# Performance work log

Measured on AMD Instinct MI355X. Metric: run time of the kernel, lower is better.

The kernel has to match this reference:

```python
import jax, jax.numpy as jnp
import numpy as np

B, N, CT, CS, CP, H, NB = 1, 1024, 768, 384, 16, 16, 4
DH = CT // H
NL, NK = 8, 32          # n_local_tokens, n_keys
K = NL + NK
SCALE = 1.0 / np.sqrt(DH)


def _ln(x, g=None, b=None, eps=1e-5):
    m = jnp.mean(x, -1, keepdims=True)
    v = jnp.var(x, -1, keepdims=True)
    y = (x - m) * jax.lax.rsqrt(v + eps)
    if g is not None:
        y = y * g
    if b is not None:
        y = y + b
    return y


def _adaln(a, s, sln_g, sw, sb, shw):
    # AF3 AdaLN: a <- sigmoid(Lin(s_n)) * LN(a) + LinNoBias(s_n)
    an = _ln(a)
    sn = _ln(s, sln_g)
    return jax.nn.sigmoid(sn @ sw + sb) * an + sn @ shw


def _indices(X_L):
    # n_local sequence neighbours (clamped window) + n_keys spatial nearest
    off = jnp.arange(NL) - NL // 2
    loc = jnp.clip(jnp.arange(N)[:, None] + off[None, :], 0, N - 1)  # [N,NL]
    d2 = jnp.sum((X_L[:, :, None, :] - X_L[:, None, :, :]) ** 2, -1)  # [B,N,N]
    _, nk = jax.lax.top_k(-d2, NK)                                    # [B,N,NK]
    loc = jnp.broadcast_to(loc[None], (X_L.shape[0], N, NL))
    return jnp.concatenate([loc, nk], -1)                             # [B,N,K]


def setup_inputs() -> dict:
    key = jax.random.key(0)
    ks = list(jax.random.split(key, 24))
    f32 = jnp.float32

    def rn(k, shape, s=0.02):
        return (jax.random.normal(k, shape) * s).astype(f32)

    d = {}
    d['A_I'] = jax.random.normal(ks[0], (B, N, CT), f32)
    d['S_I'] = jax.random.normal(ks[1], (B, N, CS), f32)
    d['Z_II'] = jax.random.normal(ks[2], (B, N, N, CP), f32)
    d['X_L'] = jax.random.normal(ks[3], (B, N, 3), f32) * 10.0
    d['f'] = jax.random.randint(ks[4], (B, N), 0, 4)
    # attention-pair-bias block params (stacked over NB blocks)
    d['aln1_sln_g'] = jnp.ones((NB, CS), f32)
    d['aln1_sw'] = rn(ks[5], (NB, CS, CT))
    d['aln1_sb'] = jnp.zeros((NB, CT), f32)
    d['aln1_shw'] = rn(ks[6], (NB, CS, CT))
    d['Wq'] = rn(ks[7], (NB, CT, CT))
    d['bq'] = jnp.zeros((NB, CT), f32)
    d['Wk'] = rn(ks[8], (NB, CT, CT))
    d['Wv'] = rn(ks[9], (NB, CT, CT))
    d['pair_ln_g'] = jnp.ones((NB, CP), f32)
    d['pair_ln_b'] = jnp.zeros((NB, CP), f32)
    d['Wb'] = rn(ks[10], (NB, CP, H))
    d['Wg'] = rn(ks[11], (NB, CT, CT))
    d['Wo'] = rn(ks[12], (NB, CT, CT))
    d['sg_w'] = rn(ks[13], (NB, CS, CT))
    d['sg_b'] = jnp.full((NB, CT), -2.0, f32)   # LinearBiasInit(-2.0)
    # conditioned transition block params
    d['aln2_sln_g'] = jnp.ones((NB, CS), f32)
    d['aln2_sw'] = rn(ks[14], (NB, CS, CT))
    d['aln2_sb'] = jnp.zeros((NB, CT), f32)
    d['aln2_shw'] = rn(ks[15], (NB, CS, CT))
    d['t_w1'] = rn(ks[16], (NB, CT, 2 * CT))
    d['t_w2'] = rn(ks[17], (NB, CT, 2 * CT))
    d['t_w3'] = rn(ks[18], (NB, 2 * CT, CT))
    d['tsg_w'] = rn(ks[19], (NB, CS, CT))
    d['tsg_b'] = jnp.full((NB, CT), -2.0, f32)
    return d


def reference(A_I, S_I, Z_II, X_L, f,
              aln1_sln_g, aln1_sw, aln1_sb, aln1_shw,
              Wq, bq, Wk, Wv, pair_ln_g, pair_ln_b, Wb, Wg, Wo, sg_w, sg_b,
              aln2_sln_g, aln2_sw, aln2_sb, aln2_shw,
              t_w1, t_w2, t_w3, tsg_w, tsg_b):
    idx = _indices(X_L)                       # [B,N,K] int
    bb = jnp.arange(B)[:, None, None]
    nn_ = jnp.arange(N)[None, :, None]
    zg = Z_II[bb, nn_, idx]                   # [B,N,K,CP] gathered pair reps
    A = A_I
    for i in range(NB):
        # LocalAttentionPairBias
        an = _adaln(A, S_I, aln1_sln_g[i], aln1_sw[i], aln1_sb[i], aln1_shw[i])
        q = (an @ Wq[i] + bq[i]).reshape(B, N, H, DH)
        kg = (an @ Wk[i])[bb, idx].reshape(B, N, K, H, DH)
        vg = (an @ Wv[i])[bb, idx].reshape(B, N, K, H, DH)
        bias = _ln(zg, pair_ln_g[i], pair_ln_b[i]) @ Wb[i]      # [B,N,K,H]
        sc = jnp.einsum('bnhd,bnkhd->bnhk', q, kg) * SCALE + jnp.swapaxes(bias, -1, -2)
        w = jax.nn.softmax(sc, -1)                               # [B,N,H,K]
        o = jnp.einsum('bnhk,bnkhd->bnhd', w, vg).reshape(B, N, CT)
        o = jax.nn.sigmoid(an @ Wg[i]) * o                       # per-channel gate
        o = jax.nn.sigmoid(S_I @ sg_w[i] + sg_b[i]) * (o @ Wo[i])
        A = A + o                                                # dropout=0 (eval)
        # ConditionedTransitionBlock (SwiGLU, n=2)
        an2 = _adaln(A, S_I, aln2_sln_g[i], aln2_sw[i], aln2_sb[i], aln2_shw[i])
        hb = jax.nn.silu(an2 @ t_w1[i]) * (an2 @ t_w2[i])
        A = A + jax.nn.sigmoid(S_I @ tsg_w[i] + tsg_b[i]) * (hb @ t_w3[i])
    return A
```

## Files before the change

### kernel.cpp

```cpp
#include <hip/hip_runtime.h>
#include <hip/hip_bf16.h>
#include <math.h>
#include <stdint.h>

#define NTOK 1024
#define CT   768
#define CS   384
#define CP   16
#define NH   16
#define DH   48
#define NBLK 4
#define NL   8
#define NKEY 32
#define KTOT 40
#define SCALE_ 0.14433756729740643f

#define WS_BLK      8257536
#define OFF_A1SW    0
#define OFF_A1SHW   294912
#define OFF_QKVG    589824
#define OFF_WO      2949120
#define OFF_SGT     3538944
#define OFF_A2SW    4128768
#define OFF_A2SHW   4423680
#define OFF_TW1     4718592
#define OFF_TW2     5898240
#define OFF_TW3     7077888

typedef __attribute__((ext_vector_type(8))) short short8;
typedef __attribute__((ext_vector_type(4))) float f32x4;
typedef __attribute__((ext_vector_type(4))) unsigned int u32x4;

#define AS1 __attribute__((address_space(1)))
#define AS3 __attribute__((address_space(3)))

__device__ __forceinline__ float sigmoidf_(float x) {
    return 1.0f / (1.0f + __expf(-x));
}
__device__ __forceinline__ float bf2f(unsigned short u) {
    union { unsigned int i; float f; } v; v.i = (unsigned int)u << 16; return v.f;
}
__device__ __forceinline__ unsigned short f2bf(float f) {
    return __bfloat16_as_ushort(__float2bfloat16(f));
}

__device__ __forceinline__ void gl_lds16(const void* g, void* l) {
    __builtin_amdgcn_global_load_lds((const AS1 void*)(uintptr_t)g,
                                     (AS3 void*)(uintptr_t)l, 16, 0, 0);
}

__global__ __launch_bounds__(256)
void topk_kernel(const float* __restrict__ X, int* __restrict__ idx) {
    const int w = threadIdx.x >> 6;
    const int l = threadIdx.x & 63;
    const int n = blockIdx.x * 4 + w;

    const float x0 = X[n * 3 + 0], x1 = X[n * 3 + 1], x2 = X[n * 3 + 2];
    float d[16];
    unsigned long long lkey = ~0ull;
#pragma unroll
    for (int j = 0; j < 16; ++j) {
        int m = j * 64 + l;
        float dx = x0 - X[m * 3 + 0];
        float dy = x1 - X[m * 3 + 1];
        float dz = x2 - X[m * 3 + 2];
        float v = dx * dx + dy * dy + dz * dz;
        d[j] = v;
        unsigned long long key =
            ((unsigned long long)__float_as_uint(v) << 32) | (unsigned int)m;
        lkey = key < lkey ? key : lkey;
    }
    if (l < NL) {
        int loc = n + l - NL / 2;
        loc = loc < 0 ? 0 : (loc > NTOK - 1 ? NTOK - 1 : loc);
        idx[n * KTOT + l] = loc;
    }

    for (int it = 0; it < NKEY; ++it) {
        unsigned long long rk = lkey;
#pragma unroll
        for (int s = 32; s > 0; s >>= 1) {
            unsigned long long o = __shfl_xor(rk, s, 64);
            rk = o < rk ? o : rk;
        }
        unsigned int win = (unsigned int)rk;
        if (l == 0) idx[n * KTOT + NL + it] = (int)win;
        if ((int)(win & 63) == l) {
            int jw = (int)(win >> 6);
            unsigned long long nk = ~0ull;
#pragma unroll
            for (int j = 0; j < 16; ++j) {
                if (j == jw) d[j] = INFINITY;
                unsigned long long key =
                    ((unsigned long long)__float_as_uint(d[j]) << 32) |
                    (unsigned int)(j * 64 + l);
                nk = key < nk ? key : nk;
            }
            lkey = nk;
        }
    }
}

__global__ __launch_bounds__(384)
void sprep_kernel(const float* __restrict__ S, const float* __restrict__ g1,
                  const float* __restrict__ g2,
                  __hip_bfloat16* __restrict__ S_bf,
                  __hip_bfloat16* __restrict__ snb) {
    int r = blockIdx.x, t = threadIdx.x;
    int wid = t >> 6, l = t & 63;
    __shared__ float ls[12];
    float v = S[r * CS + t];
    float s = v;
#pragma unroll
    for (int m = 32; m > 0; m >>= 1) s += __shfl_xor(s, m, 64);
    if (l == 0) ls[wid] = s;
    __syncthreads();
    float mean = (ls[0] + ls[1] + ls[2] + ls[3] + ls[4] + ls[5]) * (1.0f / CS);
    float d = v - mean;
    float q = d * d;
#pragma unroll
    for (int m = 32; m > 0; m >>= 1) q += __shfl_xor(q, m, 64);
    if (l == 0) ls[6 + wid] = q;
    __syncthreads();
    float rstd = rsqrtf((ls[6] + ls[7] + ls[8] + ls[9] + ls[10] + ls[11]) *
                        (1.0f / CS) + 1e-5f);
    float ln = d * rstd;
    S_bf[r * CS + t] = __float2bfloat16(v);
#pragma unroll
    for (int j = 0; j < 8; ++j) {
        const float* g = ((j & 1) ? g2 : g1) + (j >> 1) * CS;
        snb[((size_t)j * NTOK + r) * CS + t] = __float2bfloat16(ln * g[t]);
    }
}

__global__ __launch_bounds__(256)
void adaapply_kernel(const float* __restrict__ A,
                     const __hip_bfloat16* __restrict__ SIG,
                     const __hip_bfloat16* __restrict__ SH,
                     __hip_bfloat16* __restrict__ an) {
    int r = blockIdx.x, t = threadIdx.x;
    int wid = t >> 6, l = t & 63;
    __shared__ float ls[8];
    const float* ar = A + (size_t)r * CT;
    float v0 = ar[t], v1 = ar[t + 256], v2 = ar[t + 512];
    float s = v0 + v1 + v2;
#pragma unroll
    for (int m = 32; m > 0; m >>= 1) s += __shfl_xor(s, m, 64);
    if (l == 0) ls[wid] = s;
    __syncthreads();
    float mean = (ls[0] + ls[1] + ls[2] + ls[3]) * (1.0f / CT);
    float d0 = v0 - mean, d1 = v1 - mean, d2 = v2 - mean;
    float q = d0 * d0 + d1 * d1 + d2 * d2;
#pragma unroll
    for (int m = 32; m > 0; m >>= 1) q += __shfl_xor(q, m, 64);
    if (l == 0) ls[4 + wid] = q;
    __syncthreads();
    float rstd = rsqrtf((ls[4] + ls[5] + ls[6] + ls[7]) * (1.0f / CT) + 1e-5f);
    size_t base = (size_t)r * CT;
    float dd[3] = {d0, d1, d2};
#pragma unroll
    for (int k = 0; k < 3; ++k) {
        int c = t + k * 256;
        float sg = sigmoidf_(__bfloat162float(SIG[base + c]));
        float sh = __bfloat162float(SH[base + c]);
        an[base + c] = __float2bfloat16(sg * dd[k] * rstd + sh);
    }
}

struct ConvDesc { const float* src; __hip_bfloat16* dst; int K; int N; int tstart; int srcStride; };
struct ConvTable { ConvDesc e[14]; };

__global__ __launch_bounds__(256)
void convT_kernel(ConvTable tab) {
    int b = blockIdx.x;
    int ei = 0;
#pragma unroll
    for (int j = 1; j < 14; ++j) if (b >= tab.e[j].tstart) ei = j;
    ConvDesc d = tab.e[ei];
    const float* src = d.src + (size_t)blockIdx.y * d.srcStride;
    unsigned short* dst = (unsigned short*)(d.dst + (size_t)blockIdx.y * WS_BLK);
    int tt = b - d.tstart;
    int ntn = d.N / 64;
    int k0 = (tt / ntn) * 128, n0 = (tt % ntn) * 64;

    __shared__ __align__(16) unsigned int lbT[64 * 64];
    const int t = threadIdx.x;
    const int nq = (t & 15) * 4;

    f32x4 va[4], vc[4];
#pragma unroll
    for (int it = 0; it < 4; ++it) {
        int k = ((t >> 4) + it * 16) * 2;
        va[it] = *(const f32x4*)&src[(size_t)(k0 + k) * d.N + n0 + nq];
        vc[it] = *(const f32x4*)&src[(size_t)(k0 + k + 1) * d.N + n0 + nq];
    }
#pragma unroll
    for (int it = 0; it < 4; ++it) {
        int k2 = (t >> 4) + it * 16;
#pragma unroll
        for (int j = 0; j < 4; ++j) {
            int n = nq + j;
            unsigned int u = (unsigned int)f2bf(va[it][j]) |
                             ((unsigned int)f2bf(vc[it][j]) << 16);
            lbT[n * 64 + (k2 ^ (((n >> 1) & 15) << 2))] = u;
        }
    }
    __syncthreads();
#pragma unroll
    for (int it = 0; it < 4; ++it) {
        int task = t + it * 256;
        int n = task >> 4;
        int kcg = task & 15;
        int k2s = (kcg * 4) ^ (((n >> 1) & 15) << 2);
        u32x4 v = *(const u32x4*)&lbT[n * 64 + k2s];
        *(u32x4*)&dst[(size_t)(n0 + n) * d.K + k0 + kcg * 8] = v;
    }
}

__global__ __launch_bounds__(256)
void biasprep_kernel(const float* __restrict__ bq, const float* __restrict__ sg_b,
                     const float* __restrict__ tsg_b, float* __restrict__ qb,
                     float* __restrict__ sb2) {
    int t = blockIdx.x * 256 + threadIdx.x;
    if (t < NBLK * 3072) {
        int i = t / 3072, c = t % 3072;
        qb[t] = (c < 768) ? bq[i * 768 + c] : 0.0f;
    }
    if (t < NBLK * 1536) {
        int i = t / 1536, c = t % 1536;
        sb2[t] = (c < 768) ? sg_b[i * 768 + c] : tsg_b[i * 768 + c - 768];
    }
}

template <int MODE>
__global__ __launch_bounds__(256)
void gemmw_kernel(const __hip_bfloat16* A, const __hip_bfloat16* B1,
                  const float* cb1, const float* cb2,
                  __hip_bfloat16* outb, __hip_bfloat16* outb2,
                  int K, int N, int ldo) {
    __shared__ __align__(16) char As[2][16384];
    __shared__ __align__(16) char Bs[2][8192];

    const float* cb = cb1;
    __hip_bfloat16* outp = outb;
    if constexpr (MODE == 5) {
        int z = blockIdx.z;
        int j = z & 7, half = z >> 3;
        A += (size_t)j * NTOK * CS;
        B1 += (size_t)(j >> 1) * WS_BLK + ((j & 1) ? OFF_A2SW : OFF_A1SW)
            + (size_t)half * (OFF_A1SHW - OFF_A1SW);
        cb = half ? nullptr : (((j & 1) ? cb2 : cb1) + (j >> 1) * CT);
        outp = (half ? outb2 : outb) + (size_t)j * NTOK * CT;
    } else if constexpr (MODE == 6) {
        int z = blockIdx.z;
        B1 += (size_t)z * WS_BLK;
        cb = cb1 + z * 1536;
        outp = outb + (size_t)z * NTOK * 1536;
    }

    const int tid = threadIdx.x;
    const int lane = tid & 63;
    const int wid = tid >> 6;
    const int row0 = blockIdx.y * 128;
    const int col0 = blockIdx.x * 64;

    const int srow = tid >> 3;
    const int sg_e = (((tid & 7) ^ (srow & 7)) << 3);
    const __hip_bfloat16* ag = A + (size_t)(row0 + srow) * K + sg_e;
    const __hip_bfloat16* bg = B1 + (size_t)(col0 + srow) * K + sg_e;
    const size_t r32K = (size_t)32 * K;

    auto STAGE = [&](int bi) {
        char* al = As[bi] + tid * 16;
        char* bl = Bs[bi] + tid * 16;
        gl_lds16(ag, al);
        gl_lds16(ag + r32K, al + 4096);
        gl_lds16(ag + 2 * r32K, al + 8192);
        gl_lds16(ag + 3 * r32K, al + 12288);
        gl_lds16(bg, bl);
        gl_lds16(bg + r32K, bl + 4096);
        ag += 64; bg += 64;
    };

    f32x4 acc[2][4];
#pragma unroll
    for (int i = 0; i < 2; ++i)
#pragma unroll
        for (int j = 0; j < 4; ++j) acc[i][j] = (f32x4){0.f, 0.f, 0.f, 0.f};

    const int l15 = lane & 15;
    const int lhi = lane >> 4;
    const int nIter = K >> 6;

    STAGE(0);
    for (int it = 0; it < nIter; ++it) {
        __syncthreads();
        if (it + 1 < nIter) STAGE((it + 1) & 1);
        const char* Ab = As[it & 1];
        const char* Bb = Bs[it & 1];
#pragma unroll
        for (int kk = 0; kk < 2; ++kk) {
            const int c = lhi + 4 * kk;
            short8 a[2], bv[4];
#pragma unroll
            for (int mi = 0; mi < 2; ++mi) {
                int ra = wid * 32 + mi * 16 + l15;
                a[mi] = *(const short8*)(Ab + ra * 128 + (((c ^ (ra & 7)) << 4)));
            }
#pragma unroll
            for (int ni = 0; ni < 4; ++ni) {
                int rb = ni * 16 + l15;
                bv[ni] = *(const short8*)(Bb + rb * 128 + (((c ^ (rb & 7)) << 4)));
            }
#pragma unroll
            for (int mi = 0; mi < 2; ++mi)
#pragma unroll
                for (int ni = 0; ni < 4; ++ni)
                    acc[mi][ni] = __builtin_amdgcn_mfma_f32_16x16x32_bf16(
                        a[mi], bv[ni], acc[mi][ni], 0, 0, 0);
        }
    }

#pragma unroll
    for (int mi = 0; mi < 2; ++mi)
#pragma unroll
        for (int ni = 0; ni < 4; ++ni) {
            int col = col0 + ni * 16 + l15;
            int rbase = row0 + wid * 32 + mi * 16 + lhi * 4;
            float cbv = cb ? cb[col] : 0.0f;
            f32x4 v = acc[mi][ni];
#pragma unroll
            for (int r = 0; r < 4; ++r)
                outp[(size_t)(rbase + r) * ldo + col] = __float2bfloat16(v[r] + cbv);
        }
}

template <int MODE>
__global__ __launch_bounds__(256)
void gemm_kernel(const __hip_bfloat16* __restrict__ A,
                 const __hip_bfloat16* B1,
                 const __hip_bfloat16* B2,
                 const __hip_bfloat16* __restrict__ auxb, int ld_aux,
                 float* __restrict__ outf,
                 __hip_bfloat16* outb,
                 int K, int N, int ldo) {
    constexpr bool DUAL = (MODE == 2);
    __shared__ __align__(16) char As[2][8192];
    __shared__ __align__(16) char Bs[2][8192];
    __shared__ __align__(16) char Bs2[DUAL ? 2 : 1][DUAL ? 8192 : 16];

    const int tid = threadIdx.x;
    const int lane = tid & 63;
    const int wid = tid >> 6;
    const int wr = wid >> 1, wc = wid & 1;
    const int row0 = blockIdx.y * 64;
    const int col0 = blockIdx.x * 64;

    const int srow = tid >> 3;
    const int sg_e = (((tid & 7) ^ (srow & 7)) << 3);
    const __hip_bfloat16* ag = A + (size_t)(row0 + srow) * K + sg_e;
    const __hip_bfloat16* bg = B1 + (size_t)(col0 + srow) * K + sg_e;
    const __hip_bfloat16* bg2 = DUAL ? (B2 + (size_t)(col0 + srow) * K + sg_e) : nullptr;
    const size_t r32K = (size_t)32 * K;

    auto STAGE = [&](int bi) {
        gl_lds16(ag, As[bi] + tid * 16);
        gl_lds16(ag + r32K, As[bi] + 4096 + tid * 16);
        gl_lds16(bg, Bs[bi] + tid * 16);
        gl_lds16(bg + r32K, Bs[bi] + 4096 + tid * 16);
        if (DUAL) {
            gl_lds16(bg2, Bs2[bi] + tid * 16);
            gl_lds16(bg2 + r32K, Bs2[bi] + 4096 + tid * 16);
            bg2 += 64;
        }
        ag += 64; bg += 64;
    };

    f32x4 acc[2][2];
    f32x4 acc2[2][2];
#pragma unroll
    for (int i = 0; i < 2; ++i)
#pragma unroll
        for (int j = 0; j < 2; ++j) {
            acc[i][j] = (f32x4){0.f, 0.f, 0.f, 0.f};
            acc2[i][j] = (f32x4){0.f, 0.f, 0.f, 0.f};
        }

    const int l15 = lane & 15;
    const int lhi = lane >> 4;
    const int nIter = K >> 6;

    STAGE(0);
    for (int it = 0; it < nIter; ++it) {
        __syncthreads();
        if (it + 1 < nIter) STAGE((it + 1) & 1);
        const char* Ab = As[it & 1];
        const char* Bb = Bs[it & 1];
        const char* Cb = DUAL ? Bs2[it & 1] : nullptr;
#pragma unroll
        for (int kk = 0; kk < 2; ++kk) {
            const int c = lhi + 4 * kk;
            const int ra0 = wr * 32 + l15, ra1 = ra0 + 16;
            const int rb0 = wc * 32 + l15, rb1 = rb0 + 16;
            short8 a0 = *(const short8*)(Ab + ra0 * 128 + (((c ^ (ra0 & 7)) << 4)));
            short8 a1 = *(const short8*)(Ab + ra1 * 128 + (((c ^ (ra1 & 7)) << 4)));
            short8 b0 = *(const short8*)(Bb + rb0 * 128 + (((c ^ (rb0 & 7)) << 4)));
            short8 b1 = *(const short8*)(Bb + rb1 * 128 + (((c ^ (rb1 & 7)) << 4)));
            acc[0][0] = __builtin_amdgcn_mfma_f32_16x16x32_bf16(a0, b0, acc[0][0], 0, 0, 0);
            acc[0][1] = __builtin_amdgcn_mfma_f32_16x16x32_bf16(a0, b1, acc[0][1], 0, 0, 0);
            acc[1][0] = __builtin_amdgcn_mfma_f32_16x16x32_bf16(a1, b0, acc[1][0], 0, 0, 0);
            acc[1][1] = __builtin_amdgcn_mfma_f32_16x16x32_bf16(a1, b1, acc[1][1], 0, 0, 0);
            if (DUAL) {
                short8 c0 = *(const short8*)(Cb + rb0 * 128 + (((c ^ (rb0 & 7)) << 4)));
                short8 c1 = *(const short8*)(Cb + rb1 * 128 + (((c ^ (rb1 & 7)) << 4)));
                acc2[0][0] = __builtin_amdgcn_mfma_f32_16x16x32_bf16(a0, c0, acc2[0][0], 0, 0, 0);
                acc2[0][1] = __builtin_amdgcn_mfma_f32_16x16x32_bf16(a0, c1, acc2[0][1], 0, 0, 0);
                acc2[1][0] = __builtin_amdgcn_mfma_f32_16x16x32_bf16(a1, c0, acc2[1][0], 0, 0, 0);
                acc2[1][1] = __builtin_amdgcn_mfma_f32_16x16x32_bf16(a1, c1, acc2[1][1], 0, 0, 0);
            }
        }
    }

#pragma unroll
    for (int mi = 0; mi < 2; ++mi)
#pragma unroll
        for (int ni = 0; ni < 2; ++ni) {
            f32x4 v1 = acc[mi][ni];
            f32x4 v2 = acc2[mi][ni];
            int col = col0 + wc * 32 + ni * 16 + l15;
            int rbase = row0 + wr * 32 + mi * 16 + lhi * 4;
#pragma unroll
            for (int r = 0; r < 4; ++r) {
                int row = rbase + r;
                size_t o = (size_t)row * ldo + col;
                if (MODE == 2) {
                    float x = v1[r];
                    outb[o] = __float2bfloat16(x * sigmoidf_(x) * v2[r]);
                } else {
                    float g = sigmoidf_(__bfloat162float(auxb[(size_t)row * ld_aux + col]));
                    outf[o] += g * v1[r];
                }
            }
        }
}

__global__ __launch_bounds__(256)
void attn_kernel(const __hip_bfloat16* __restrict__ qkvg,
                 const float* __restrict__ Z,
                 const int* __restrict__ idx,
                 const float* __restrict__ pg, const float* __restrict__ pb,
                 const float* __restrict__ Wbp,
                 __hip_bfloat16* __restrict__ o2) {
    int n = blockIdx.x;
    int t = threadIdx.x;
    __shared__ __align__(16) unsigned short qs[768];
    __shared__ float sc[16][48];
    __shared__ float lnz[KTOT][16];
    __shared__ float wb[16][17];
    __shared__ float pgs[16], pbs[16];
    __shared__ int sidx[KTOT];

    wb[t >> 4][t & 15] = Wbp[t];
    if (t < 96) ((short8*)qs)[t] = ((const short8*)(qkvg + (size_t)n * 3072))[t];
    if (t >= 96 && t < 96 + KTOT) sidx[t - 96] = idx[n * KTOT + (t - 96)];
    if (t >= 160 && t < 176) pgs[t - 160] = pg[t - 160];
    if (t >= 176 && t < 192) pbs[t - 176] = pb[t - 176];
    __syncthreads();

    if (t < KTOT) {
        const f32x4* z = (const f32x4*)(Z + ((size_t)n * NTOK + sidx[t]) * CP);
        f32x4 z0 = z[0], z1 = z[1], z2 = z[2], z3 = z[3];
        float v[16];
#pragma unroll
        for (int e = 0; e < 4; ++e) { v[e] = z0[e]; v[4 + e] = z1[e]; v[8 + e] = z2[e]; v[12 + e] = z3[e]; }
        float s = 0.0f;
#pragma unroll
        for (int c = 0; c < 16; ++c) s += v[c];
        float mean = s * (1.0f / 16.0f);
        float s2 = 0.0f;
#pragma unroll
        for (int c = 0; c < 16; ++c) { float d = v[c] - mean; s2 += d * d; }
        float rstd = rsqrtf(s2 * (1.0f / 16.0f) + 1e-5f);
#pragma unroll
        for (int c = 0; c < 16; ++c) lnz[t][c] = (v[c] - mean) * rstd * pgs[c] + pbs[c];
    }
    __syncthreads();

    for (int task = t; task < NH * KTOT; task += 256) {
        int h = task / KTOT, k = task - h * KTOT;
        const short8* kp = (const short8*)((const unsigned short*)qkvg +
                                           (size_t)sidx[k] * 3072 + 768 + h * DH);
        const short8* qp = (const short8*)(qs + h * DH);
        float s = 0.0f;
#pragma unroll
        for (int j = 0; j < 6; ++j) {
            short8 kv = kp[j];
            short8 qv = qp[j];
#pragma unroll
            for (int e = 0; e < 8; ++e)
                s += bf2f((unsigned short)qv[e]) * bf2f((unsigned short)kv[e]);
        }
        float bias = 0.0f;
#pragma unroll
        for (int c = 0; c < 16; ++c) bias += lnz[k][c] * wb[c][h];
        sc[h][k] = s * SCALE_ + bias;
    }
    __syncthreads();

    {
        int h = t >> 4, l = t & 15;
        float v0 = sc[h][l];
        float v1 = sc[h][l + 16];
        float v2 = (l < 8) ? sc[h][l + 32] : -INFINITY;
        float mx = fmaxf(fmaxf(v0, v1), v2);
#pragma unroll
        for (int m = 8; m > 0; m >>= 1) mx = fmaxf(mx, __shfl_xor(mx, m, 16));
        float e0 = __expf(v0 - mx), e1 = __expf(v1 - mx);
        float e2 = (l < 8) ? __expf(v2 - mx) : 0.0f;
        float sm = e0 + e1 + e2;
#pragma unroll
        for (int m = 8; m > 0; m >>= 1) sm += __shfl_xor(sm, m, 16);
        float inv = 1.0f / sm;
        sc[h][l] = e0 * inv;
        sc[h][l + 16] = e1 * inv;
        if (l < 8) sc[h][l + 32] = e2 * inv;
    }
    __syncthreads();

    if (t < 96) {
        int h = t / 6, c6 = t - h * 6;
        int d0 = c6 * 8;
        const unsigned short* vbase = (const unsigned short*)qkvg + 1536 + h * DH + d0;
        float acc[8] = {0, 0, 0, 0, 0, 0, 0, 0};
        for (int k = 0; k < KTOT; ++k) {
            short8 vv = *(const short8*)(vbase + (size_t)sidx[k] * 3072);
            float w = sc[h][k];
#pragma unroll
            for (int e = 0; e < 8; ++e) acc[e] += w * bf2f((unsigned short)vv[e]);
        }
        short8 gv = *(const short8*)((const unsigned short*)qkvg +
                                     (size_t)n * 3072 + 2304 + h * DH + d0);
        short8 ov;
#pragma unroll
        for (int e = 0; e < 8; ++e) {
            float g = sigmoidf_(bf2f((unsigned short)gv[e]));
            ov[e] = (short)f2bf(g * acc[e]);
        }
        *(short8*)((unsigned short*)o2 + (size_t)n * CT + h * DH + d0) = ov;
    }
}

extern "C" void kernel_launch(void* const* d_in, const int* in_sizes, int n_in,
                              void* d_out, int out_size, void* d_ws, size_t ws_size,
                              hipStream_t stream) {
    const float* A_I  = (const float*)d_in[0];
    const float* S_I  = (const float*)d_in[1];
    const float* Z_II = (const float*)d_in[2];
    const float* X_L  = (const float*)d_in[3];
    const float* aln1_sln_g = (const float*)d_in[5];
    const float* aln1_sw    = (const float*)d_in[6];
    const float* aln1_sb    = (const float*)d_in[7];
    const float* aln1_shw   = (const float*)d_in[8];
    const float* Wq  = (const float*)d_in[9];
    const float* bq  = (const float*)d_in[10];
    const float* Wk  = (const float*)d_in[11];
    const float* Wv  = (const float*)d_in[12];
    const float* pair_ln_g = (const float*)d_in[13];
    const float* pair_ln_b = (const float*)d_in[14];
    const float* Wbp = (const float*)d_in[15];
    const float* Wg  = (const float*)d_in[16];
    const float* Wo  = (const float*)d_in[17];
    const float* sg_w = (const float*)d_in[18];
    const float* sg_b = (const float*)d_in[19];
    const float* aln2_sln_g = (const float*)d_in[20];
    const float* aln2_sw    = (const float*)d_in[21];
    const float* aln2_sb    = (const float*)d_in[22];
    const float* aln2_shw   = (const float*)d_in[23];
    const float* t_w1 = (const float*)d_in[24];
    const float* t_w2 = (const float*)d_in[25];
    const float* t_w3 = (const float*)d_in[26];
    const float* tsg_w = (const float*)d_in[27];
    const float* tsg_b = (const float*)d_in[28];
    (void)in_sizes; (void)n_in; (void)out_size; (void)ws_size;

    float* A = (float*)d_out;

    char* ws = (char*)d_ws;
    size_t off = 0;
    auto alloc = [&](size_t bytes) {
        void* p = ws + off;
        off += (bytes + 255) & ~(size_t)255;
        return p;
    };
    int*   idx    = (int*)  alloc(NTOK * KTOT * 4);
    __hip_bfloat16* S_bf  = (__hip_bfloat16*)alloc((size_t)NTOK * CS * 2);
    __hip_bfloat16* snb   = (__hip_bfloat16*)alloc((size_t)8 * NTOK * CS * 2);
    __hip_bfloat16* an    = (__hip_bfloat16*)alloc((size_t)NTOK * CT * 2);
    __hip_bfloat16* qkvg  = (__hip_bfloat16*)alloc((size_t)NTOK * 3072 * 2);
    __hip_bfloat16* sgateb= (__hip_bfloat16*)alloc((size_t)NBLK * NTOK * 1536 * 2);
    __hip_bfloat16* SIG   = (__hip_bfloat16*)alloc((size_t)8 * NTOK * CT * 2);
    __hip_bfloat16* SH    = (__hip_bfloat16*)alloc((size_t)8 * NTOK * CT * 2);
    __hip_bfloat16* o2    = (__hip_bfloat16*)alloc((size_t)NTOK * CT * 2);
    __hip_bfloat16* hb    = (__hip_bfloat16*)alloc((size_t)NTOK * 2 * CT * 2);
    float* qkvgbias = (float*)alloc((size_t)NBLK * 3072 * 4);
    float* sgbias   = (float*)alloc((size_t)NBLK * 1536 * 4);
    __hip_bfloat16* Wbuf = (__hip_bfloat16*)alloc((size_t)NBLK * WS_BLK * 2);

    hipMemcpyAsync(A, A_I, (size_t)NTOK * CT * 4, hipMemcpyDeviceToDevice, stream);

    topk_kernel<<<NTOK / 4, 256, 0, stream>>>(X_L, idx);
    sprep_kernel<<<NTOK, 384, 0, stream>>>(S_I, aln1_sln_g, aln2_sln_g, S_bf, snb);
    biasprep_kernel<<<NBLK * 3072 / 256, 256, 0, stream>>>(bq, sg_b, tsg_b, qkvgbias, sgbias);

    {
        ConvTable tab;
        int p = 0, ts = 0;
        auto add = [&](const float* s, size_t dstOff, int Kk, int Nn, int sstride) {
            tab.e[p].src = s; tab.e[p].dst = Wbuf + dstOff; tab.e[p].K = Kk;
            tab.e[p].N = Nn; tab.e[p].tstart = ts; tab.e[p].srcStride = sstride;
            ts += (Kk / 128) * (Nn / 64); ++p;
        };
        add(aln1_sw,  OFF_A1SW,           384, 768,  CS * CT);
        add(aln1_shw, OFF_A1SHW,          384, 768,  CS * CT);
        add(Wq, OFF_QKVG + 0 * 589824,    768, 768,  CT * CT);
        add(Wk, OFF_QKVG + 1 * 589824,    768, 768,  CT * CT);
        add(Wv, OFF_QKVG + 2 * 589824,    768, 768,  CT * CT);
        add(Wg, OFF_QKVG + 3 * 589824,    768, 768,  CT * CT);
        add(Wo, OFF_WO,                   768, 768,  CT * CT);
        add(sg_w,  OFF_SGT,               384, 768,  CS * CT);
        add(tsg_w, OFF_SGT + 768 * 384,   384, 768,  CS * CT);
        add(aln2_sw,  OFF_A2SW,           384, 768,  CS * CT);
        add(aln2_shw, OFF_A2SHW,          384, 768,  CS * CT);
        add(t_w1, OFF_TW1,                768, 1536, CT * 2 * CT);
        add(t_w2, OFF_TW2,                768, 1536, CT * 2 * CT);
        add(t_w3, OFF_TW3,                1536, 768, 2 * CT * CT);
        convT_kernel<<<dim3(ts, NBLK), 256, 0, stream>>>(tab);
    }

    gemmw_kernel<5><<<dim3(12, 8, 16), 256, 0, stream>>>(
        snb, Wbuf, aln1_sb, aln2_sb, SIG, SH, 384, 768, 768);
    gemmw_kernel<6><<<dim3(24, 8, 4), 256, 0, stream>>>(
        S_bf, Wbuf + OFF_SGT, sgbias, nullptr, sgateb, nullptr, 384, 1536, 1536);

    for (int i = 0; i < NBLK; ++i) {
        const __hip_bfloat16* Wb_i = Wbuf + (size_t)i * WS_BLK;
        __hip_bfloat16* sg_i = sgateb + (size_t)i * NTOK * 1536;

        adaapply_kernel<<<NTOK, 256, 0, stream>>>(
            A, SIG + (size_t)(2 * i) * NTOK * CT, SH + (size_t)(2 * i) * NTOK * CT, an);
        gemmw_kernel<4><<<dim3(48, 8), 256, 0, stream>>>(
            an, Wb_i + OFF_QKVG, qkvgbias + (size_t)i * 3072, nullptr,
            qkvg, nullptr, 768, 3072, 3072);
        attn_kernel<<<NTOK, 256, 0, stream>>>(
            qkvg, Z_II, idx, pair_ln_g + (size_t)i * CP, pair_ln_b + (size_t)i * CP,
            Wbp + (size_t)i * CP * NH, o2);
        gemm_kernel<3><<<dim3(12, 16), 256, 0, stream>>>(
            o2, Wb_i + OFF_WO, nullptr, sg_i, 1536, A, nullptr, 768, 768, 768);

        adaapply_kernel<<<NTOK, 256, 0, stream>>>(
            A, SIG + (size_t)(2 * i + 1) * NTOK * CT, SH + (size_t)(2 * i + 1) * NTOK * CT, an);
        gemm_kernel<2><<<dim3(24, 16), 256, 0, stream>>>(
            an, Wb_i + OFF_TW1, Wb_i + OFF_TW2, nullptr, 0, nullptr, hb, 768, 1536, 1536);
        gemm_kernel<3><<<dim3(12, 16), 256, 0, stream>>>(
            hb, Wb_i + OFF_TW3, nullptr, sg_i + 768, 1536, A, nullptr, 1536, 768, 768);
    }
}
```

Measured before the change: 411.9 us.

## Fuse prep kernels, transpose weights in registers, split attention V-sum across threads

Merges the topk, S layernorm prep and bias prep kernels into one launch that dispatches on block index, removing two kernel launches. Rewrites the weight transpose/convert kernel to do an 8x8 register transpose per thread with 128x128 tiles, dropping the LDS staging buffer and its barrier. Splits the attention value accumulation over 40 keys across two thread groups (192 threads), combining the partial sums through shared memory, which doubles parallelism in that loop at the cost of an extra barrier and LDS traffic.

Result: no change. 407.7 us (-1.0%).

```diff
diff --git a/kernel.cpp b/kernel.cpp
--- a/kernel.cpp
+++ b/kernel.cpp
@@ -29,7 +29,6 @@
 
 typedef __attribute__((ext_vector_type(8))) short short8;
 typedef __attribute__((ext_vector_type(4))) float f32x4;
-typedef __attribute__((ext_vector_type(4))) unsigned int u32x4;
 
 #define AS1 __attribute__((address_space(1)))
 #define AS3 __attribute__((address_space(3)))
@@ -49,87 +48,112 @@
                                      (AS3 void*)(uintptr_t)l, 16, 0, 0);
 }
 
-__global__ __launch_bounds__(256)
-void topk_kernel(const float* __restrict__ X, int* __restrict__ idx) {
-    const int w = threadIdx.x >> 6;
-    const int l = threadIdx.x & 63;
-    const int n = blockIdx.x * 4 + w;
-
-    const float x0 = X[n * 3 + 0], x1 = X[n * 3 + 1], x2 = X[n * 3 + 2];
-    float d[16];
-    unsigned long long lkey = ~0ull;
-#pragma unroll
-    for (int j = 0; j < 16; ++j) {
-        int m = j * 64 + l;
-        float dx = x0 - X[m * 3 + 0];
-        float dy = x1 - X[m * 3 + 1];
-        float dz = x2 - X[m * 3 + 2];
-        float v = dx * dx + dy * dy + dz * dz;
-        d[j] = v;
-        unsigned long long key =
-            ((unsigned long long)__float_as_uint(v) << 32) | (unsigned int)m;
-        lkey = key < lkey ? key : lkey;
-    }
-    if (l < NL) {
-        int loc = n + l - NL / 2;
-        loc = loc < 0 ? 0 : (loc > NTOK - 1 ? NTOK - 1 : loc);
-        idx[n * KTOT + l] = loc;
-    }
-
-    for (int it = 0; it < NKEY; ++it) {
-        unsigned long long rk = lkey;
-#pragma unroll
-        for (int s = 32; s > 0; s >>= 1) {
-            unsigned long long o = __shfl_xor(rk, s, 64);
-            rk = o < rk ? o : rk;
-        }
-        unsigned int win = (unsigned int)rk;
-        if (l == 0) idx[n * KTOT + NL + it] = (int)win;
-        if ((int)(win & 63) == l) {
-            int jw = (int)(win >> 6);
-            unsigned long long nk = ~0ull;
-#pragma unroll
-            for (int j = 0; j < 16; ++j) {
-                if (j == jw) d[j] = INFINITY;
-                unsigned long long key =
-                    ((unsigned long long)__float_as_uint(d[j]) << 32) |
-                    (unsigned int)(j * 64 + l);
-                nk = key < nk ? key : nk;
+struct PrepArgs {
+    const float* X_L; int* idx;
+    const float* S; const float* g1; const float* g2;
+    __hip_bfloat16* S_bf; __hip_bfloat16* snb;
+    const float* bq; const float* sg_b; const float* tsg_b;
+    float* qb; float* sb2;
+};
+
+__global__ __launch_bounds__(384)
+void prep_kernel(PrepArgs pa) {
+    __shared__ float ls[12];
+    const int t = threadIdx.x;
+    const int b = blockIdx.x;
+
+    if (b < 256) {
+        const int w = t >> 6;
+        if (w >= 4) return;
+        const int l = t & 63;
+        const int n = b * 4 + w;
+        const float* X = pa.X_L;
+        int* idx = pa.idx;
+
+        const float x0 = X[n * 3 + 0], x1 = X[n * 3 + 1], x2 = X[n * 3 + 2];
+        float d[16];
+        unsigned long long lkey = ~0ull;
+#pragma unroll
+        for (int j = 0; j < 16; ++j) {
+            int m = j * 64 + l;
+            float dx = x0 - X[m * 3 + 0];
+            float dy = x1 - X[m * 3 + 1];
+            float dz = x2 - X[m * 3 + 2];
+            float v = dx * dx + dy * dy + dz * dz;
+            d[j] = v;
+            unsigned long long key =
+                ((unsigned long long)__float_as_uint(v) << 32) | (unsigned int)m;
+            lkey = key < lkey ? key : lkey;
+        }
+        if (l < NL) {
+            int loc = n + l - NL / 2;
+            loc = loc < 0 ? 0 : (loc > NTOK - 1 ? NTOK - 1 : loc);
+            idx[n * KTOT + l] = loc;
+        }
+        for (int it = 0; it < NKEY; ++it) {
+            unsigned long long rk = lkey;
+#pragma unroll
+            for (int s = 32; s > 0; s >>= 1) {
+                unsigned long long o = __shfl_xor(rk, s, 64);
+                rk = o < rk ? o : rk;
             }
-            lkey = nk;
-        }
-    }
-}
-
-__global__ __launch_bounds__(384)
-void sprep_kernel(const float* __restrict__ S, const float* __restrict__ g1,
-                  const float* __restrict__ g2,
-                  __hip_bfloat16* __restrict__ S_bf,
-                  __hip_bfloat16* __restrict__ snb) {
-    int r = blockIdx.x, t = threadIdx.x;
-    int wid = t >> 6, l = t & 63;
-    __shared__ float ls[12];
-    float v = S[r * CS + t];
-    float s = v;
-#pragma unroll
-    for (int m = 32; m > 0; m >>= 1) s += __shfl_xor(s, m, 64);
-    if (l == 0) ls[wid] = s;
-    __syncthreads();
-    float mean = (ls[0] + ls[1] + ls[2] + ls[3] + ls[4] + ls[5]) * (1.0f / CS);
-    float d = v - mean;
-    float q = d * d;
-#pragma unroll
-    for (int m = 32; m > 0; m >>= 1) q += __shfl_xor(q, m, 64);
-    if (l == 0) ls[6 + wid] = q;
-    __syncthreads();
-    float rstd = rsqrtf((ls[6] + ls[7] + ls[8] + ls[9] + ls[10] + ls[11]) *
-                        (1.0f / CS) + 1e-5f);
-    float ln = d * rstd;
-    S_bf[r * CS + t] = __float2bfloat16(v);
-#pragma unroll
-    for (int j = 0; j < 8; ++j) {
-        const float* g = ((j & 1) ? g2 : g1) + (j >> 1) * CS;
-        snb[((size_t)j * NTOK + r) * CS + t] = __float2bfloat16(ln * g[t]);
+            unsigned int win = (unsigned int)rk;
+            if (l == 0) idx[n * KTOT + NL + it] = (int)win;
+            if ((int)(win & 63) == l) {
+                int jw = (int)(win >> 6);
+                unsigned long long nk = ~0ull;
+#pragma unroll
+                for (int j = 0; j < 16; ++j) {
+                    if (j == jw) d[j] = INFINITY;
+                    unsigned long long key =
+                        ((unsigned long long)__float_as_uint(d[j]) << 32) |
+                        (unsigned int)(j * 64 + l);
+                    nk = key < nk ? key : nk;
+                }
+                lkey = nk;
+            }
+        }
+        return;
+    }
+
+    if (b < 1280) {
+        int r = b - 256;
+        int wid = t >> 6, l = t & 63;
+        float v = pa.S[r * CS + t];
+        float s = v;
+#pragma unroll
+        for (int m = 32; m > 0; m >>= 1) s += __shfl_xor(s, m, 64);
+        if (l == 0) ls[wid] = s;
+        __syncthreads();
+        float mean = (ls[0] + ls[1] + ls[2] + ls[3] + ls[4] + ls[5]) * (1.0f / CS);
+        float d = v - mean;
+        float q = d * d;
+#pragma unroll
+        for (int m = 32; m > 0; m >>= 1) q += __shfl_xor(q, m, 64);
+        if (l == 0) ls[6 + wid] = q;
+        __syncthreads();
+        float rstd = rsqrtf((ls[6] + ls[7] + ls[8] + ls[9] + ls[10] + ls[11]) *
+                            (1.0f / CS) + 1e-5f);
+        float ln = d * rstd;
+        pa.S_bf[r * CS + t] = __float2bfloat16(v);
+#pragma unroll
+        for (int j = 0; j < 8; ++j) {
+            const float* g = ((j & 1) ? pa.g2 : pa.g1) + (j >> 1) * CS;
+            pa.snb[((size_t)j * NTOK + r) * CS + t] = __float2bfloat16(ln * g[t]);
+        }
+        return;
+    }
+
+    {
+        int tt = (b - 1280) * 384 + t;
+        if (tt < NBLK * 3072) {
+            int i = tt / 3072, c = tt % 3072;
+            pa.qb[tt] = (c < 768) ? pa.bq[i * 768 + c] : 0.0f;
+        }
+        if (tt < NBLK * 1536) {
+            int i = tt / 1536, c = tt % 1536;
+            pa.sb2[tt] = (c < 768) ? pa.sg_b[i * 768 + c] : pa.tsg_b[i * 768 + c - 768];
+        }
     }
 }
 
@@ -180,55 +204,29 @@
     const float* src = d.src + (size_t)blockIdx.y * d.srcStride;
     unsigned short* dst = (unsigned short*)(d.dst + (size_t)blockIdx.y * WS_BLK);
     int tt = b - d.tstart;
-    int ntn = d.N / 64;
-    int k0 = (tt / ntn) * 128, n0 = (tt % ntn) * 64;
-
-    __shared__ __align__(16) unsigned int lbT[64 * 64];
-    const int t = threadIdx.x;
-    const int nq = (t & 15) * 4;
-
-    f32x4 va[4], vc[4];
-#pragma unroll
-    for (int it = 0; it < 4; ++it) {
-        int k = ((t >> 4) + it * 16) * 2;
-        va[it] = *(const f32x4*)&src[(size_t)(k0 + k) * d.N + n0 + nq];
-        vc[it] = *(const f32x4*)&src[(size_t)(k0 + k + 1) * d.N + n0 + nq];
-    }
-#pragma unroll
-    for (int it = 0; it < 4; ++it) {
-        int k2 = (t >> 4) + it * 16;
-#pragma unroll
-        for (int j = 0; j < 4; ++j) {
-            int n = nq + j;
-            unsigned int u = (unsigned int)f2bf(va[it][j]) |
-                             ((unsigned int)f2bf(vc[it][j]) << 16);
-            lbT[n * 64 + (k2 ^ (((n >> 1) & 15) << 2))] = u;
-        }
-    }
-    __syncthreads();
-#pragma unroll
-    for (int it = 0; it < 4; ++it) {
-        int task = t + it * 256;
-        int n = task >> 4;
-        int kcg = task & 15;
-        int k2s = (kcg * 4) ^ (((n >> 1) & 15) << 2);
-        u32x4 v = *(const u32x4*)&lbT[n * 64 + k2s];
-        *(u32x4*)&dst[(size_t)(n0 + n) * d.K + k0 + kcg * 8] = v;
-    }
-}
-
-__global__ __launch_bounds__(256)
-void biasprep_kernel(const float* __restrict__ bq, const float* __restrict__ sg_b,
-                     const float* __restrict__ tsg_b, float* __restrict__ qb,
-                     float* __restrict__ sb2) {
-    int t = blockIdx.x * 256 + threadIdx.x;
-    if (t < NBLK * 3072) {
-        int i = t / 3072, c = t % 3072;
-        qb[t] = (c < 768) ? bq[i * 768 + c] : 0.0f;
-    }
-    if (t < NBLK * 1536) {
-        int i = t / 1536, c = t % 1536;
-        sb2[t] = (c < 768) ? sg_b[i * 768 + c] : tsg_b[i * 768 + c - 768];
+    int ntn = d.N / 128;
+    int k0 = (tt / ntn) * 128, n0 = (tt % ntn) * 128;
+
+    const int ck = threadIdx.x & 15;
+    const int cn = threadIdx.x >> 4;
+
+    const float* sp = src + (size_t)(k0 + ck * 8) * d.N + n0 + cn * 8;
+    f32x4 va[8], vb[8];
+#pragma unroll
+    for (int r = 0; r < 8; ++r) {
+        va[r] = *(const f32x4*)(sp + (size_t)r * d.N);
+        vb[r] = *(const f32x4*)(sp + (size_t)r * d.N + 4);
+    }
+    unsigned short* dp = dst + (size_t)(n0 + cn * 8) * d.K + k0 + ck * 8;
+#pragma unroll
+    for (int j = 0; j < 8; ++j) {
+        short8 o;
+#pragma unroll
+        for (int e = 0; e < 8; ++e) {
+            float f = (j < 4) ? va[e][j] : vb[e][j - 4];
+            o[e] = (short)f2bf(f);
+        }
+        *(short8*)(dp + (size_t)j * d.K) = o;
     }
 }
 
@@ -459,6 +457,7 @@
     __shared__ float wb[16][17];
     __shared__ float pgs[16], pbs[16];
     __shared__ int sidx[KTOT];
+    __shared__ float pacc[96][8];
 
     wb[t >> 4][t & 15] = Wbp[t];
     if (t < 96) ((short8*)qs)[t] = ((const short8*)(qkvg + (size_t)n * 3072))[t];
@@ -527,24 +526,35 @@
     }
     __syncthreads();
 
+    float acc[8] = {0, 0, 0, 0, 0, 0, 0, 0};
+    const int half = (t >= 96) ? 1 : 0;
+    const int tt = t - half * 96;
+    if (t < 192) {
+        int h = tt / 6, c6 = tt - h * 6;
+        int d0 = c6 * 8;
+        const unsigned short* vbase = (const unsigned short*)qkvg + 1536 + h * DH + d0;
+        for (int k = half * 20; k < half * 20 + 20; ++k) {
+            short8 vv = *(const short8*)(vbase + (size_t)sidx[k] * 3072);
+            float w = sc[h][k];
+#pragma unroll
+            for (int e = 0; e < 8; ++e) acc[e] += w * bf2f((unsigned short)vv[e]);
+        }
+    }
+    if (half && t < 192) {
+#pragma unroll
+        for (int e = 0; e < 8; ++e) pacc[tt][e] = acc[e];
+    }
+    __syncthreads();
     if (t < 96) {
         int h = t / 6, c6 = t - h * 6;
         int d0 = c6 * 8;
-        const unsigned short* vbase = (const unsigned short*)qkvg + 1536 + h * DH + d0;
-        float acc[8] = {0, 0, 0, 0, 0, 0, 0, 0};
-        for (int k = 0; k < KTOT; ++k) {
-            short8 vv = *(const short8*)(vbase + (size_t)sidx[k] * 3072);
-            float w = sc[h][k];
-#pragma unroll
-            for (int e = 0; e < 8; ++e) acc[e] += w * bf2f((unsigned short)vv[e]);
-        }
         short8 gv = *(const short8*)((const unsigned short*)qkvg +
                                      (size_t)n * 3072 + 2304 + h * DH + d0);
         short8 ov;
 #pragma unroll
         for (int e = 0; e < 8; ++e) {
             float g = sigmoidf_(bf2f((unsigned short)gv[e]));
-            ov[e] = (short)f2bf(g * acc[e]);
+            ov[e] = (short)f2bf(g * (acc[e] + pacc[t][e]));
         }
         *(short8*)((unsigned short*)o2 + (size_t)n * CT + h * DH + d0) = ov;
     }
@@ -608,9 +618,15 @@
 
     hipMemcpyAsync(A, A_I, (size_t)NTOK * CT * 4, hipMemcpyDeviceToDevice, stream);
 
-    topk_kernel<<<NTOK / 4, 256, 0, stream>>>(X_L, idx);
-    sprep_kernel<<<NTOK, 384, 0, stream>>>(S_I, aln1_sln_g, aln2_sln_g, S_bf, snb);
-    biasprep_kernel<<<NBLK * 3072 / 256, 256, 0, stream>>>(bq, sg_b, tsg_b, qkvgbias, sgbias);
+    {
+        PrepArgs pa;
+        pa.X_L = X_L; pa.idx = idx;
+        pa.S = S_I; pa.g1 = aln1_sln_g; pa.g2 = aln2_sln_g;
+        pa.S_bf = S_bf; pa.snb = snb;
+        pa.bq = bq; pa.sg_b = sg_b; pa.tsg_b = tsg_b;
+        pa.qb = qkvgbias; pa.sb2 = sgbias;
+        prep_kernel<<<1312, 384, 0, stream>>>(pa);
+    }
 
     {
         ConvTable tab;
@@ -618,7 +634,7 @@
         auto add = [&](const float* s, size_t dstOff, int Kk, int Nn, int sstride) {
             tab.e[p].src = s; tab.e[p].dst = Wbuf + dstOff; tab.e[p].K = Kk;
             tab.e[p].N = Nn; tab.e[p].tstart = ts; tab.e[p].srcStride = sstride;
-            ts += (Kk / 128) * (Nn / 64); ++p;
+            ts += (Kk / 128) * (Nn / 128); ++p;
         };
         add(aln1_sw,  OFF_A1SW,           384, 768,  CS * CT);
         add(aln1_shw, OFF_A1SHW,          384, 768,  CS * CT);
```
